# Kernel optimization log

Measured on AMD Instinct MI355X. Metric: run time of the kernel, lower is better.

The kernel has to match this reference:

```python
import jax, jax.numpy as jnp
import numpy as np

NUM_HEADS = 8
KEY_DIM = 512  # d_gain = 1/sqrt(key_dim) in the original (NOT per-head dim)
MASK_FILL = -1000000.0


def setup_inputs() -> dict:
    key = jax.random.key(0)
    ks = jax.random.split(key, 6)
    N, Tq, Tk, D, U = 8, 1024, 1024, 512, 512
    query = jax.random.normal(ks[0], (N, Tq, D), dtype=jnp.float32)
    key_t = jax.random.normal(ks[1], (N, Tk, D), dtype=jnp.float32)
    key_mask = jax.random.randint(ks[2], (N, Tk), 0, 2).astype(bool)
    Wq = jax.random.normal(ks[3], (D, U), dtype=jnp.float32) / np.sqrt(D)
    Wk = jax.random.normal(ks[4], (D, U), dtype=jnp.float32) / np.sqrt(D)
    Wv = jax.random.normal(ks[5], (D, U), dtype=jnp.float32) / np.sqrt(D)
    return {"query": query, "key": key_t, "key_mask": key_mask,
            "Wq": Wq, "Wk": Wk, "Wv": Wv}


def reference(query, key, key_mask, Wq, Wk, Wv):
    N, Tq, _ = query.shape
    Tk = key.shape[1]
    U = Wq.shape[1]
    h = NUM_HEADS
    d = U // h
    scale = 1.0 / (KEY_DIM ** 0.5)

    # projections then split heads: [N,T,U] -> [h,N,T,d]
    q = (query @ Wq).reshape(N, Tq, h, d).transpose(2, 0, 1, 3)
    k = (key @ Wk).reshape(N, Tk, h, d).transpose(2, 0, 1, 3)
    v = (key @ Wv).reshape(N, Tk, h, d).transpose(2, 0, 1, 3)

    scores = scale * jnp.einsum('hnqd,hnkd->hnqk', q, k)
    scores = jnp.where(key_mask[None, :, None, :], scores, MASK_FILL)
    attn = jax.nn.softmax(scores, axis=3)
    out = jnp.einsum('hnqk,hnkd->hnqd', attn, v)
    # merge heads: [h,N,Tq,d] -> [N,Tq,h*d]
    return out.transpose(1, 2, 0, 3).reshape(N, Tq, U)
```

## Files before the change

kernel.cpp:

```cpp
#include <hip/hip_runtime.h>
#include <hip/hip_bf16.h>

typedef unsigned short u16;
typedef __attribute__((ext_vector_type(8))) short short8;
typedef __attribute__((ext_vector_type(4))) short short4v;
typedef __attribute__((ext_vector_type(4))) float f32x4;

#define NB 8
#define TT 1024
#define DD 512
#define UU 512
#define HH 8
#define DH 64
#define SCALE 0.044194173824159216f
#define LOG2E 1.4426950408889634f
#define MASK_FILL_2 -1442695.0f

__device__ __forceinline__ float ld_flex(const void* p, long i, bool f32) {
  if (f32) return ((const float*)p)[i];
  unsigned int u = (unsigned int)(((const u16*)p)[i]) << 16;
  return __uint_as_float(u);
}

__device__ __forceinline__ u16 f32_to_bf16(float f) {
  unsigned int u = __float_as_uint(f);
  unsigned int r = (u + 0x7FFFu + ((u >> 16) & 1u)) >> 16;
  return (u16)r;
}

__device__ __forceinline__ float ex2(float x) {
#if __has_builtin(__builtin_amdgcn_exp2f)
  return __builtin_amdgcn_exp2f(x);
#else
  return __expf(x * 0.6931471805599453f);
#endif
}

__device__ __forceinline__ unsigned int pk_bf16(float a, float b) {
  union { __hip_bfloat162 h2; unsigned int u; } c;
  c.h2 = __float22bfloat162_rn(make_float2(a, b));
  return c.u;
}

__device__ __forceinline__ void gld16(const void* g, void* l) {
  __builtin_amdgcn_global_load_lds(
      (const __attribute__((address_space(1))) unsigned int*)g,
      (__attribute__((address_space(3))) unsigned int*)l, 16, 0, 0);
}

#define CONV_BLOCKS 8192
#define WT_BLOCKS 768
#define MASK_BLOCKS 32

__global__ __launch_bounds__(256) void prep_kernel(
    const void* __restrict__ query, const void* __restrict__ key,
    const void* __restrict__ W0, const void* __restrict__ W1,
    const void* __restrict__ W2, const void* __restrict__ mask,
    u16* __restrict__ Xq, u16* __restrict__ Xk, u16* __restrict__ Wt,
    float* __restrict__ maskadd, int* __restrict__ flags) {
  __shared__ float tile[32][33];
  __shared__ int s_f32, s_mi32;
  const int b = blockIdx.x, tid = threadIdx.x;

  if (tid == 0) { s_f32 = 0; s_mi32 = 1; }
  __syncthreads();
  {
    const u16* qh = (const u16*)query;
    int weird = 0;
#pragma unroll
    for (int p = 0; p < 4; ++p) {
      unsigned int u = (unsigned int)qh[tid * 4 + p] << 16;
      float v = __uint_as_float(u);
      if (!(v == v) || fabsf(v) > 1e6f) weird = 1;
    }
    if (weird) atomicOr(&s_f32, 1);
    const unsigned int* mi = (const unsigned int*)mask;
    if (mi[tid * 2] > 1u || mi[tid * 2 + 1] > 1u) atomicAnd(&s_mi32, 0);
  }
  __syncthreads();
  const bool f32 = s_f32 != 0;
  const bool mi32 = s_mi32 != 0;
  if (b == CONV_BLOCKS && tid == 0) { flags[0] = s_f32; flags[1] = s_mi32; }

  if (b < CONV_BLOCKS) {
    if (!f32) return;
    const void* in = (b < 4096) ? query : key;
    u16* out = (b < 4096) ? Xq : Xk;
    int i = (b & 4095) * 256 + tid;
    float4 v = ((const float4*)in)[i];
    ushort4 o;
    o.x = f32_to_bf16(v.x); o.y = f32_to_bf16(v.y);
    o.z = f32_to_bf16(v.z); o.w = f32_to_bf16(v.w);
    ((ushort4*)out)[i] = o;
  } else if (b < CONV_BLOCKS + WT_BLOCKS) {
    const int lb = b - CONV_BLOCKS;
    const int z = lb >> 8, rem = lb & 255;
    const int k0 = (rem & 15) * 32, n0 = (rem >> 4) * 32;
    const void* W = (z == 0) ? W0 : (z == 1) ? W1 : W2;
    const float sc = (z == 0) ? SCALE * LOG2E : 1.0f;
    u16* out = Wt + (size_t)z * DD * UU;
#pragma unroll
    for (int p = 0; p < 4; ++p) {
      int i = (tid >> 5) + p * 8, j = tid & 31;
      tile[i][j] = ld_flex(W, (long)(k0 + i) * UU + n0 + j, f32);
    }
    __syncthreads();
#pragma unroll
    for (int p = 0; p < 4; ++p) {
      int nl = (tid >> 5) + p * 8, kl = tid & 31;
      out[(size_t)(n0 + nl) * DD + k0 + kl] = f32_to_bf16(tile[kl][nl] * sc);
    }
  } else {
    const int i = (b - CONV_BLOCKS - WT_BLOCKS) * 256 + tid;
    bool mv = mi32 ? (((const int*)mask)[i] != 0)
                   : (((const unsigned char*)mask)[i] != 0);
    maskadd[i] = mv ? 0.0f : MASK_FILL_2;
  }
}

__global__ __launch_bounds__(256) void proj_mfma(
    const void* __restrict__ query, const void* __restrict__ key,
    const u16* __restrict__ Xq, const u16* __restrict__ Xk,
    const u16* __restrict__ Wt, u16* __restrict__ Qp, u16* __restrict__ Kp,
    u16* __restrict__ Vt, const int* __restrict__ flags) {
  __shared__ __align__(16) u16 smem[128 * 136];
  const bool f32 = flags[0] != 0;
  const int lid = blockIdx.x + (blockIdx.y << 6) + (blockIdx.z << 8);
  const int swz = (lid & 7) * 96 + (lid >> 3);
  const int bx = swz & 63, by = (swz >> 6) & 3, z = swz >> 8;
  const u16* X = (z == 0) ? (f32 ? Xq : (const u16*)query)
                          : (f32 ? Xk : (const u16*)key);
  const u16* Wz = Wt + (size_t)z * DD * UU;
  const int m0 = bx * 128, n0 = by * 128;
  const int tid = threadIdx.x;
  const int w = tid >> 6, l = tid & 63;
  const int quad = l >> 4, l15 = l & 15;
  const int wm = (w >> 1) * 64, wn = (w & 1) * 64;

  const int c0 = w * 128 + l;
  const int row0 = c0 >> 2, q0 = (c0 & 3) * 8;
  const int c1 = c0 + 64;
  const int row1 = c1 >> 2, q1 = (c1 & 3) * 8;
  const u16* aS0 = X + (size_t)(m0 + row0) * DD + q0;
  const u16* aS1 = X + (size_t)(m0 + row1) * DD + q1;
  const u16* bS0 = Wz + (size_t)(n0 + row0) * DD + q0;
  const u16* bS1 = Wz + (size_t)(n0 + row1) * DD + q1;
  const int dD0 = w * 1024;
  const int dD1 = w * 1024 + 512;

  f32x4 acc[4][4];
#pragma unroll
  for (int mi = 0; mi < 4; ++mi)
#pragma unroll
    for (int ni = 0; ni < 4; ++ni)
#pragma unroll
      for (int r = 0; r < 4; ++r) acc[mi][ni][r] = 0.0f;

  gld16(aS0, smem + dD0);
  gld16(aS1, smem + dD1);
  gld16(bS0, smem + 4096 + dD0);
  gld16(bS1, smem + 4096 + dD1);

#pragma unroll 1
  for (int t = 0; t < 16; ++t) {
    const int co = (t & 1) * 8192;
    if (t < 15) {
      const int k1 = (t + 1) * 32;
      const int no = ((t + 1) & 1) * 8192;
      gld16(aS0 + k1, smem + no + dD0);
      gld16(aS1 + k1, smem + no + dD1);
      gld16(bS0 + k1, smem + no + 4096 + dD0);
      gld16(bS1 + k1, smem + no + 4096 + dD1);
      asm volatile("s_waitcnt vmcnt(4)" ::: "memory");
    } else {
      asm volatile("s_waitcnt vmcnt(0)" ::: "memory");
    }
    __builtin_amdgcn_s_barrier();

    short8 af[4], bf[4];
#pragma unroll
    for (int mi = 0; mi < 4; ++mi)
      af[mi] = *(const short8*)&smem[co + (wm + mi * 16 + l15) * 32 + quad * 8];
#pragma unroll
    for (int ni = 0; ni < 4; ++ni)
      bf[ni] = *(const short8*)&smem[co + 4096 + (wn + ni * 16 + l15) * 32 + quad * 8];
#pragma unroll
    for (int mi = 0; mi < 4; ++mi)
#pragma unroll
      for (int ni = 0; ni < 4; ++ni)
        acc[mi][ni] = __builtin_amdgcn_mfma_f32_16x16x32_bf16(
            af[mi], bf[ni], acc[mi][ni], 0, 0, 0);
    __builtin_amdgcn_s_barrier();
  }

  if (z < 2) {
#pragma unroll
    for (int mi = 0; mi < 4; ++mi)
#pragma unroll
      for (int ni = 0; ni < 4; ++ni) {
        const int ml = wm + mi * 16 + quad * 4;
        const int nl = wn + ni * 16 + l15;
#pragma unroll
        for (int r = 0; r < 4; ++r)
          smem[(ml + r) * 136 + nl] = f32_to_bf16(acc[mi][ni][r]);
      }
  } else {
#pragma unroll
    for (int mi = 0; mi < 4; ++mi)
#pragma unroll
      for (int ni = 0; ni < 4; ++ni) {
        const int ml = wm + mi * 16 + quad * 4;
        const int nl = wn + ni * 16 + l15;
        ushort4 pk;
        pk.x = f32_to_bf16(acc[mi][ni][0]);
        pk.y = f32_to_bf16(acc[mi][ni][1]);
        pk.z = f32_to_bf16(acc[mi][ni][2]);
        pk.w = f32_to_bf16(acc[mi][ni][3]);
        *(ushort4*)&smem[nl * 136 + ml] = pk;
      }
  }
  __syncthreads();

  if (z < 2) {
    u16* outp = (z == 0) ? Qp : Kp;
#pragma unroll
    for (int p = 0; p < 8; ++p) {
      const int idx = tid + p * 256;
      const int row = idx >> 4, c8 = (idx & 15) * 8;
      short8 v = *(const short8*)&smem[row * 136 + c8];
      *(short8*)&outp[(size_t)(m0 + row) * UU + n0 + c8] = v;
    }
  } else {
    const int nb = m0 >> 10, tk0 = m0 & 1023;
#pragma unroll
    for (int p = 0; p < 8; ++p) {
      const int idx = tid + p * 256;
      const int row = idx >> 4, c8 = (idx & 15) * 8;
      const int u = n0 + row, h = u >> 6, dh = u & 63;
      short8 v = *(const short8*)&smem[row * 136 + c8];
      *(short8*)&Vt[(size_t)((nb * HH + h) * DH + dh) * TT + tk0 + c8] = v;
    }
  }
}

__global__ __launch_bounds__(256, 4) void attn_mfma(
    const u16* __restrict__ Qp, const u16* __restrict__ Kp,
    const u16* __restrict__ Vt, const float* __restrict__ maskadd,
    void* __restrict__ out, const int* __restrict__ flags) {
  __shared__ __align__(16) char smem[25344];
  u16* sU = (u16*)smem;
  const int tid = threadIdx.x;
  const int w = tid >> 6, l = tid & 63;
  const int quad = l >> 4, l15 = l & 15;
  const int lid = blockIdx.x + (blockIdx.y << 4) + (blockIdx.z << 7);
  const int swz = (lid & 7) * 128 + (lid >> 3);
  const int qt = swz & 15, h = (swz >> 4) & 7, n = swz >> 7;
  const int q0 = qt * 64;
  const bool f32o = flags[0] != 0;
  u16* Pw = sU + 8192 + w * 576;
  float* s_mask = (float*)(smem + 20992);
  float* lp = (float*)(smem + 25088);

  ((float4*)s_mask)[tid] = ((const float4*)(maskadd + n * TT))[tid];

  const u16* qbase = Qp + (size_t)(n * TT + q0 + w * 16 + l15) * UU + h * DH + quad * 8;
  short8 bq[2];
  bq[0] = *(const short8*)(qbase);
  bq[1] = *(const short8*)(qbase + 32);

  const int lr3 = l >> 3, ls7 = l & 7;
  const int lr2 = l >> 2, ls3 = l & 3;
  const u16* kcur = Kp + (size_t)(n * TT + w * 8 + lr3) * UU + h * DH +
                    ((ls7 ^ lr3) * 8);
  const u16* vcur = Vt + (size_t)((n * HH + h) * DH + w * 16 + lr2) * TT +
                    ((ls3 ^ (lr2 & 3)) * 8);

  f32x4 o[4];
  float lsum = 0.0f;
#pragma unroll
  for (int ni = 0; ni < 4; ++ni)
#pragma unroll
    for (int r = 0; r < 4; ++r) o[ni][r] = 0.0f;

  __syncthreads();

  gld16(kcur, smem + w * 1024);
  gld16(vcur, smem + 8192 + w * 1024);

#pragma unroll 1
  for (int t = 0; t < 32; ++t) {
    const int co = (t & 1) * 2048;
    if (t < 31) {
      const int no = ((t + 1) & 1) * 4096;
      gld16(kcur + (size_t)(t + 1) * 32 * UU, smem + no + w * 1024);
      gld16(vcur + (t + 1) * 32, smem + 8192 + no + w * 1024);
      asm volatile("s_waitcnt vmcnt(2)" ::: "memory");
    } else {
      asm volatile("s_waitcnt vmcnt(0)" ::: "memory");
    }
    __builtin_amdgcn_s_barrier();

    const int kb = t * 32;
    short8 ak[2][2];
#pragma unroll
    for (int kt = 0; kt < 2; ++kt)
#pragma unroll
      for (int kd = 0; kd < 2; ++kd)
        ak[kt][kd] = *(const short8*)&sU[co + (kt * 16 + l15) * 64 +
                                         (((kd * 4 + quad) ^ (l15 & 7)) * 8)];
    float4 mk0 = *(const float4*)&s_mask[kb + quad * 4];
    float4 mk1 = *(const float4*)&s_mask[kb + 16 + quad * 4];

    f32x4 s[2];
#pragma unroll
    for (int kt = 0; kt < 2; ++kt) {
#pragma unroll
      for (int r = 0; r < 4; ++r) s[kt][r] = 0.0f;
#pragma unroll
      for (int kd = 0; kd < 2; ++kd)
        s[kt] = __builtin_amdgcn_mfma_f32_16x16x32_bf16(
            ak[kt][kd], bq[kd], s[kt], 0, 0, 0);
    }

#pragma unroll
    for (int kt = 0; kt < 2; ++kt) {
      const float4 mk = kt ? mk1 : mk0;
      float e0 = ex2(s[kt][0] + mk.x);
      float e1 = ex2(s[kt][1] + mk.y);
      float e2 = ex2(s[kt][2] + mk.z);
      float e3 = ex2(s[kt][3] + mk.w);
      lsum += (e0 + e1) + (e2 + e3);
      uint2 pk = make_uint2(pk_bf16(e0, e1), pk_bf16(e2, e3));
      *(uint2*)&Pw[l15 * 36 + kt * 16 + quad * 4] = pk;
    }

    short8 vf[4];
#pragma unroll
    for (int ni = 0; ni < 4; ++ni)
      vf[ni] = *(const short8*)&sU[4096 + co + (ni * 16 + l15) * 32 +
                                   ((quad ^ (l15 & 3)) * 8)];

    short8 ap;
    {
      short4v lo = *(const short4v*)&Pw[l15 * 36 + quad * 8];
      short4v hi = *(const short4v*)&Pw[l15 * 36 + quad * 8 + 4];
      union { short8 v8; short4v v4[2]; } u;
      u.v4[0] = lo; u.v4[1] = hi;
      ap = u.v8;
    }

#pragma unroll
    for (int ni = 0; ni < 4; ++ni)
      o[ni] = __builtin_amdgcn_mfma_f32_16x16x32_bf16(ap, vf[ni], o[ni], 0, 0, 0);

    __builtin_amdgcn_s_barrier();
  }

  lsum += __shfl_xor(lsum, 16);
  lsum += __shfl_xor(lsum, 32);
  if (l < 16) lp[w * 16 + l] = lsum;
  __syncthreads();

  float den[4];
#pragma unroll
  for (int r = 0; r < 4; ++r) den[r] = lp[w * 16 + quad * 4 + r];

#pragma unroll
  for (int ni = 0; ni < 4; ++ni)
#pragma unroll
    for (int r = 0; r < 4; ++r) {
      const int q = q0 + w * 16 + quad * 4 + r;
      const float v = o[ni][r] / den[r];
      const size_t idx = (size_t)(n * TT + q) * UU + h * DH + ni * 16 + l15;
      if (f32o) ((float*)out)[idx] = v;
      else ((u16*)out)[idx] = f32_to_bf16(v);
    }
}

extern "C" void kernel_launch(void* const* d_in, const int* in_sizes, int n_in,
                              void* d_out, int out_size, void* d_ws, size_t ws_size,
                              hipStream_t stream) {
  const void* query = d_in[0];
  const void* key   = d_in[1];
  const void* mask  = d_in[2];
  const void* Wq    = d_in[3];
  const void* Wk    = d_in[4];
  const void* Wv    = d_in[5];

  char* base = (char*)d_ws;
  int* flags = (int*)base;
  float* maskadd = (float*)(base + 256);
  u16* Wt  = (u16*)(base + 64 * 1024);
  u16* Xq  = Wt + (size_t)3 * DD * UU;
  u16* Xk  = Xq + (size_t)NB * TT * DD;
  u16* Qp  = Xk + (size_t)NB * TT * DD;
  u16* Kp  = Qp + (size_t)NB * TT * UU;
  u16* Vtp = Kp + (size_t)NB * TT * UU;

  prep_kernel<<<CONV_BLOCKS + WT_BLOCKS + MASK_BLOCKS, 256, 0, stream>>>(
      query, key, Wq, Wk, Wv, mask, Xq, Xk, Wt, maskadd, flags);

  dim3 pgrid(NB * TT / 128, UU / 128, 3);
  proj_mfma<<<pgrid, 256, 0, stream>>>(query, key, Xq, Xk, Wt, Qp, Kp, Vtp, flags);

  dim3 agrid(TT / 64, HH, NB);
  attn_mfma<<<agrid, 256, 0, stream>>>(Qp, Kp, Vtp, maskadd, d_out, flags);
}
```

Before: 149.9 us.

## Double K/V tile size in attention loop, store mask as bf16, add setprio

The attention kernel now loads 64-key K/V tiles per iteration instead of 32, halving loop trips and barriers, and processes each tile as two 32-key sub-steps. The mask is kept in shared memory as bf16, and MFMA sections are wrapped in s_setprio to favour matrix issue across waves. The prep kernel's fp32->bf16 conversion uses a quarter as many blocks, each handling four elements per thread. Larger LDS use (about 39KB) may lower occupancy under the 4-blocks launch bound.

```diff
diff --git a/kernel.cpp b/kernel.cpp
--- a/kernel.cpp
+++ b/kernel.cpp
@@ -48,7 +48,7 @@
       (__attribute__((address_space(3))) unsigned int*)l, 16, 0, 0);
 }
 
-#define CONV_BLOCKS 8192
+#define CONV_BLOCKS 2048
 #define WT_BLOCKS 768
 #define MASK_BLOCKS 32
 
@@ -84,14 +84,18 @@
 
   if (b < CONV_BLOCKS) {
     if (!f32) return;
-    const void* in = (b < 4096) ? query : key;
-    u16* out = (b < 4096) ? Xq : Xk;
-    int i = (b & 4095) * 256 + tid;
-    float4 v = ((const float4*)in)[i];
-    ushort4 o;
-    o.x = f32_to_bf16(v.x); o.y = f32_to_bf16(v.y);
-    o.z = f32_to_bf16(v.z); o.w = f32_to_bf16(v.w);
-    ((ushort4*)out)[i] = o;
+#pragma unroll
+    for (int p = 0; p < 4; ++p) {
+      const int i = b * 256 + tid + p * (CONV_BLOCKS * 256);
+      const void* in = (i < 1048576) ? query : key;
+      u16* outp = (i < 1048576) ? Xq : Xk;
+      const int j = i & 1048575;
+      float4 v = ((const float4*)in)[j];
+      ushort4 o;
+      o.x = f32_to_bf16(v.x); o.y = f32_to_bf16(v.y);
+      o.z = f32_to_bf16(v.z); o.w = f32_to_bf16(v.w);
+      ((ushort4*)outp)[j] = o;
+    }
   } else if (b < CONV_BLOCKS + WT_BLOCKS) {
     const int lb = b - CONV_BLOCKS;
     const int z = lb >> 8, rem = lb & 255;
@@ -247,7 +251,7 @@
     const u16* __restrict__ Qp, const u16* __restrict__ Kp,
     const u16* __restrict__ Vt, const float* __restrict__ maskadd,
     void* __restrict__ out, const int* __restrict__ flags) {
-  __shared__ __align__(16) char smem[25344];
+  __shared__ __align__(16) char smem[39680];
   u16* sU = (u16*)smem;
   const int tid = threadIdx.x;
   const int w = tid >> 6, l = tid & 63;
@@ -257,23 +261,26 @@
   const int qt = swz & 15, h = (swz >> 4) & 7, n = swz >> 7;
   const int q0 = qt * 64;
   const bool f32o = flags[0] != 0;
-  u16* Pw = sU + 8192 + w * 576;
-  float* s_mask = (float*)(smem + 20992);
-  float* lp = (float*)(smem + 25088);
-
-  ((float4*)s_mask)[tid] = ((const float4*)(maskadd + n * TT))[tid];
+  u16* Pw = sU + 16384 + w * 576;
+  u16* s_mask = sU + 18688;
+  float* lp = (float*)(smem + 39424);
+
+  {
+    float4 m4 = ((const float4*)(maskadd + n * TT))[tid];
+    ushort4 mu;
+    mu.x = f32_to_bf16(m4.x); mu.y = f32_to_bf16(m4.y);
+    mu.z = f32_to_bf16(m4.z); mu.w = f32_to_bf16(m4.w);
+    ((ushort4*)s_mask)[tid] = mu;
+  }
 
   const u16* qbase = Qp + (size_t)(n * TT + q0 + w * 16 + l15) * UU + h * DH + quad * 8;
   short8 bq[2];
   bq[0] = *(const short8*)(qbase);
   bq[1] = *(const short8*)(qbase + 32);
 
-  const int lr3 = l >> 3, ls7 = l & 7;
-  const int lr2 = l >> 2, ls3 = l & 3;
-  const u16* kcur = Kp + (size_t)(n * TT + w * 8 + lr3) * UU + h * DH +
-                    ((ls7 ^ lr3) * 8);
-  const u16* vcur = Vt + (size_t)((n * HH + h) * DH + w * 16 + lr2) * TT +
-                    ((ls3 ^ (lr2 & 3)) * 8);
+  const int lr = l >> 3, ls = l & 7;
+  const u16* kc = Kp + (size_t)(n * TT + w * 16 + lr) * UU + h * DH + ((ls ^ lr) * 8);
+  const u16* vc = Vt + (size_t)((n * HH + h) * DH + w * 16 + lr) * TT + ((ls ^ lr) * 8);
 
   f32x4 o[4];
   float lsum = 0.0f;
@@ -284,74 +291,85 @@
 
   __syncthreads();
 
-  gld16(kcur, smem + w * 1024);
-  gld16(vcur, smem + 8192 + w * 1024);
+  gld16(kc, smem + w * 2048);
+  gld16(kc + 8 * UU, smem + w * 2048 + 1024);
+  gld16(vc, smem + 16384 + w * 2048);
+  gld16(vc + 8 * TT, smem + 16384 + w * 2048 + 1024);
 
 #pragma unroll 1
-  for (int t = 0; t < 32; ++t) {
-    const int co = (t & 1) * 2048;
-    if (t < 31) {
-      const int no = ((t + 1) & 1) * 4096;
-      gld16(kcur + (size_t)(t + 1) * 32 * UU, smem + no + w * 1024);
-      gld16(vcur + (t + 1) * 32, smem + 8192 + no + w * 1024);
-      asm volatile("s_waitcnt vmcnt(2)" ::: "memory");
+  for (int t = 0; t < 16; ++t) {
+    const int co = (t & 1) * 4096;
+    if (t < 15) {
+      const int no = ((t + 1) & 1) * 8192;
+      const u16* kn = kc + (size_t)(t + 1) * 64 * UU;
+      const u16* vn = vc + (t + 1) * 64;
+      gld16(kn, smem + no + w * 2048);
+      gld16(kn + 8 * UU, smem + no + w * 2048 + 1024);
+      gld16(vn, smem + 16384 + no + w * 2048);
+      gld16(vn + 8 * TT, smem + 16384 + no + w * 2048 + 1024);
+      asm volatile("s_waitcnt vmcnt(4)" ::: "memory");
     } else {
       asm volatile("s_waitcnt vmcnt(0)" ::: "memory");
     }
     __builtin_amdgcn_s_barrier();
 
-    const int kb = t * 32;
-    short8 ak[2][2];
-#pragma unroll
-    for (int kt = 0; kt < 2; ++kt)
-#pragma unroll
-      for (int kd = 0; kd < 2; ++kd)
-        ak[kt][kd] = *(const short8*)&sU[co + (kt * 16 + l15) * 64 +
-                                         (((kd * 4 + quad) ^ (l15 & 7)) * 8)];
-    float4 mk0 = *(const float4*)&s_mask[kb + quad * 4];
-    float4 mk1 = *(const float4*)&s_mask[kb + 16 + quad * 4];
-
-    f32x4 s[2];
-#pragma unroll
-    for (int kt = 0; kt < 2; ++kt) {
-#pragma unroll
-      for (int r = 0; r < 4; ++r) s[kt][r] = 0.0f;
-#pragma unroll
-      for (int kd = 0; kd < 2; ++kd)
-        s[kt] = __builtin_amdgcn_mfma_f32_16x16x32_bf16(
-            ak[kt][kd], bq[kd], s[kt], 0, 0, 0);
-    }
-
-#pragma unroll
-    for (int kt = 0; kt < 2; ++kt) {
-      const float4 mk = kt ? mk1 : mk0;
-      float e0 = ex2(s[kt][0] + mk.x);
-      float e1 = ex2(s[kt][1] + mk.y);
-      float e2 = ex2(s[kt][2] + mk.z);
-      float e3 = ex2(s[kt][3] + mk.w);
-      lsum += (e0 + e1) + (e2 + e3);
-      uint2 pk = make_uint2(pk_bf16(e0, e1), pk_bf16(e2, e3));
-      *(uint2*)&Pw[l15 * 36 + kt * 16 + quad * 4] = pk;
-    }
-
-    short8 vf[4];
-#pragma unroll
-    for (int ni = 0; ni < 4; ++ni)
-      vf[ni] = *(const short8*)&sU[4096 + co + (ni * 16 + l15) * 32 +
-                                   ((quad ^ (l15 & 3)) * 8)];
-
-    short8 ap;
-    {
-      short4v lo = *(const short4v*)&Pw[l15 * 36 + quad * 8];
-      short4v hi = *(const short4v*)&Pw[l15 * 36 + quad * 8 + 4];
-      union { short8 v8; short4v v4[2]; } u;
-      u.v4[0] = lo; u.v4[1] = hi;
-      ap = u.v8;
-    }
-
-#pragma unroll
-    for (int ni = 0; ni < 4; ++ni)
-      o[ni] = __builtin_amdgcn_mfma_f32_16x16x32_bf16(ap, vf[ni], o[ni], 0, 0, 0);
+#pragma unroll
+    for (int ss = 0; ss < 2; ++ss) {
+      short8 ak[2][2];
+#pragma unroll
+      for (int ktl = 0; ktl < 2; ++ktl)
+#pragma unroll
+        for (int kd = 0; kd < 2; ++kd)
+          ak[ktl][kd] = *(const short8*)&sU[co + (ss * 32 + ktl * 16 + l15) * 64 +
+                                            (((kd * 4 + quad) ^ (l15 & 7)) * 8)];
+
+      f32x4 s[2];
+      __builtin_amdgcn_s_setprio(1);
+#pragma unroll
+      for (int ktl = 0; ktl < 2; ++ktl) {
+#pragma unroll
+        for (int r = 0; r < 4; ++r) s[ktl][r] = 0.0f;
+#pragma unroll
+        for (int kd = 0; kd < 2; ++kd)
+          s[ktl] = __builtin_amdgcn_mfma_f32_16x16x32_bf16(
+              ak[ktl][kd], bq[kd], s[ktl], 0, 0, 0);
+      }
+      __builtin_amdgcn_s_setprio(0);
+
+      const int kb = t * 64 + ss * 32;
+#pragma unroll
+      for (int ktl = 0; ktl < 2; ++ktl) {
+        ushort4 mku = *(const ushort4*)&s_mask[kb + ktl * 16 + quad * 4];
+        float e0 = ex2(s[ktl][0] + __uint_as_float((unsigned)mku.x << 16));
+        float e1 = ex2(s[ktl][1] + __uint_as_float((unsigned)mku.y << 16));
+        float e2 = ex2(s[ktl][2] + __uint_as_float((unsigned)mku.z << 16));
+        float e3 = ex2(s[ktl][3] + __uint_as_float((unsigned)mku.w << 16));
+        lsum += (e0 + e1) + (e2 + e3);
+        uint2 pk = make_uint2(pk_bf16(e0, e1), pk_bf16(e2, e3));
+        *(uint2*)&Pw[l15 * 36 + ktl * 16 + quad * 4] = pk;
+      }
+
+      short8 vf[4];
+#pragma unroll
+      for (int ni = 0; ni < 4; ++ni)
+        vf[ni] = *(const short8*)&sU[8192 + co + (ni * 16 + l15) * 64 +
+                                     (((ss * 4 + quad) ^ (l15 & 7)) * 8)];
+
+      short8 ap;
+      {
+        short4v lo = *(const short4v*)&Pw[l15 * 36 + quad * 8];
+        short4v hi = *(const short4v*)&Pw[l15 * 36 + quad * 8 + 4];
+        union { short8 v8; short4v v4[2]; } u;
+        u.v4[0] = lo; u.v4[1] = hi;
+        ap = u.v8;
+      }
+
+      __builtin_amdgcn_s_setprio(1);
+#pragma unroll
+      for (int ni = 0; ni < 4; ++ni)
+        o[ni] = __builtin_amdgcn_mfma_f32_16x16x32_bf16(ap, vf[ni], o[ni], 0, 0, 0);
+      __builtin_amdgcn_s_setprio(0);
+    }
 
     __builtin_amdgcn_s_barrier();
   }
```

Result: no change. 151.2 us (+0.9%).
